# Kernel tuning notes

Hardware: AMD Instinct MI355X
Metric: run time of the kernel (lower is better)

## Reference

```python
import jax, jax.numpy as jnp
import numpy as np

B, T, H, NH, EL = 64, 1024, 256, 4, 768
DH = H // NH
EPS = 1e-3


def _ln(x, g, b):
    mu = jnp.mean(x, axis=-1, keepdims=True)
    var = jnp.var(x, axis=-1, keepdims=True)
    return (x - mu) * jax.lax.rsqrt(var + EPS) * g + b


def _glu(x, W, b):
    y = x @ W.T + b
    a, gate = jnp.split(y, 2, axis=-1)
    return a * jax.nn.sigmoid(gate)


def setup_inputs() -> dict:
    key = jax.random.key(0)
    ks = iter(jax.random.split(key, 40))
    w = lambda *s: jax.random.normal(next(ks), s, jnp.float32) * 0.02
    inp = {
        "temporal_features": jax.random.normal(next(ks), (B, T, H), jnp.float32),
        "ce": jax.random.normal(next(ks), (B, H), jnp.float32),
        # enrichment GRN (with context)
        "eg_Wa": w(H, H), "eg_ba": jnp.zeros((H,), jnp.float32),
        "eg_Wc": w(H, H),
        "eg_Wi": w(H, H), "eg_bi": jnp.zeros((H,), jnp.float32),
        "eg_Wg": w(2 * H, H), "eg_bg": jnp.zeros((2 * H,), jnp.float32),
        "eg_lng": jnp.ones((H,), jnp.float32), "eg_lnb": jnp.zeros((H,), jnp.float32),
        # interpretable MHA
        "att_Wqkv": w((2 * NH + 1) * DH, H),
        "att_Wout": w(H, DH),
        # attention gate + LN
        "ag_W": w(2 * H, H), "ag_b": jnp.zeros((2 * H,), jnp.float32),
        "aln_g": jnp.ones((H,), jnp.float32), "aln_b": jnp.zeros((H,), jnp.float32),
        # positionwise GRN (no context)
        "pg_Wa": w(H, H), "pg_ba": jnp.zeros((H,), jnp.float32),
        "pg_Wi": w(H, H), "pg_bi": jnp.zeros((H,), jnp.float32),
        "pg_Wg": w(2 * H, H), "pg_bg": jnp.zeros((2 * H,), jnp.float32),
        "pg_lng": jnp.ones((H,), jnp.float32), "pg_lnb": jnp.zeros((H,), jnp.float32),
        # decoder gate + LN
        "dg_W": w(2 * H, H), "dg_b": jnp.zeros((2 * H,), jnp.float32),
        "dln_g": jnp.ones((H,), jnp.float32), "dln_b": jnp.zeros((H,), jnp.float32),
    }
    return inp


def _forward(temporal_features, ce,
             eg_Wa, eg_ba, eg_Wc, eg_Wi, eg_bi, eg_Wg, eg_bg, eg_lng, eg_lnb,
             att_Wqkv, att_Wout,
             ag_W, ag_b, aln_g, aln_b,
             pg_Wa, pg_ba, pg_Wi, pg_bi, pg_Wg, pg_bg, pg_lng, pg_lnb,
             dg_W, dg_b, dln_g, dln_b):
    # enrichment GRN: linear + context -> ELU -> linear -> GLU -> residual -> LN
    x = temporal_features @ eg_Wa.T + eg_ba + (ce @ eg_Wc.T)[:, None, :]
    x = jax.nn.elu(x)
    x = x @ eg_Wi.T + eg_bi
    x = _glu(x, eg_Wg, eg_bg)
    enriched = _ln(x + temporal_features, eg_lng, eg_lnb)

    # interpretable multi-head attention (shared V, head-averaged output)
    qkv = enriched @ att_Wqkv.T  # [B,T,(2*NH+1)*DH]
    q = qkv[..., : NH * DH].reshape(B, T, NH, DH)
    k = qkv[..., NH * DH: 2 * NH * DH].reshape(B, T, NH, DH)
    v = qkv[..., 2 * NH * DH:]  # [B,T,DH]
    scale = DH ** -0.5
    scores = jnp.einsum("bthd,bshd->bhts", q, k) * scale  # [B,NH,T,T]
    mask = jnp.triu(jnp.full((T, T), -jnp.inf, jnp.float32), k=1)
    probs = jax.nn.softmax(scores + mask, axis=-1)
    attn_vec = jnp.einsum("bhts,bsd->bhtd", probs, v)  # [B,NH,T,DH]
    m_attn = jnp.mean(attn_vec, axis=1)  # [B,T,DH]
    a = m_attn @ att_Wout.T  # [B,T,H]

    # slice to decoder steps
    a = a[:, EL:, :]
    tf_dec = temporal_features[:, EL:, :]
    enr_dec = enriched[:, EL:, :]

    x = _glu(a, ag_W, ag_b)
    x = _ln(x + enr_dec, aln_g, aln_b)

    # positionwise GRN
    y = jax.nn.elu(x @ pg_Wa.T + pg_ba)
    y = y @ pg_Wi.T + pg_bi
    y = _glu(y, pg_Wg, pg_bg)
    x = _ln(y + x, pg_lng, pg_lnb)

    x = _glu(x, dg_W, dg_b)
    x = _ln(x + tf_dec, dln_g, dln_b)
    return x


def reference(temporal_features, ce,
              eg_Wa, eg_ba, eg_Wc, eg_Wi, eg_bi, eg_Wg, eg_bg, eg_lng, eg_lnb,
              att_Wqkv, att_Wout,
              ag_W, ag_b, aln_g, aln_b,
              pg_Wa, pg_ba, pg_Wi, pg_bi, pg_Wg, pg_bg, pg_lng, pg_lnb,
              dg_W, dg_b, dln_g, dln_b):
    return _forward(temporal_features, ce,
                    eg_Wa, eg_ba, eg_Wc, eg_Wi, eg_bi, eg_Wg, eg_bg, eg_lng, eg_lnb,
                    att_Wqkv, att_Wout,
                    ag_W, ag_b, aln_g, aln_b,
                    pg_Wa, pg_ba, pg_Wi, pg_bi, pg_Wg, pg_bg, pg_lng, pg_lnb,
                    dg_W, dg_b, dln_g, dln_b)
```

## Files before the change

### kernel.cpp

```cpp
#include <hip/hip_runtime.h>
#include <hip/hip_bf16.h>
#include <math.h>

typedef __hip_bfloat16 bf16;
typedef unsigned short u16;
typedef unsigned int u32;
typedef __attribute__((ext_vector_type(8))) short bfrag8;
typedef __attribute__((ext_vector_type(8))) _Float16 hfrag8;
typedef __attribute__((ext_vector_type(4))) float f32x4;

constexpr int Bb = 64, Tt = 1024, Hh = 256, NHn = 4, DHd = 64, ELe = 768;
constexpr int TD = Tt - ELe;
constexpr int BT = Bb * Tt;
constexpr int BD = Bb * TD;

__device__ __forceinline__ bool probe_bf16(const void* probe) {
    return *(const unsigned int*)probe == 0x3F803F80u;
}
__device__ __forceinline__ float bfbits2f(unsigned short u) {
    union { unsigned int i; float f; } c; c.i = ((unsigned int)u) << 16; return c.f;
}
__device__ __forceinline__ u16 f2bf(float f) {
    union { float f; unsigned int u; } c; c.f = f;
    unsigned int r = c.u + 0x7fffu + ((c.u >> 16) & 1u);
    return (u16)(r >> 16);
}
__device__ __forceinline__ u16 f2h(float f) {
    union { _Float16 h; u16 u; } c; c.h = (_Float16)f; return c.u;
}
__device__ __forceinline__ float h2f(u16 u) {
    union { u16 u; _Float16 h; } c; c.u = u; return (float)c.h;
}
__device__ __forceinline__ float4 load4dt(const void* p, long idx, bool bf) {
    if (bf) {
        ushort4 u = *(const ushort4*)((const unsigned short*)p + idx);
        return make_float4(bfbits2f(u.x), bfbits2f(u.y), bfbits2f(u.z), bfbits2f(u.w));
    }
    return *(const float4*)((const float*)p + idx);
}
__device__ __forceinline__ float load1dt(const void* p, long idx, bool bf) {
    return bf ? bfbits2f(((const unsigned short*)p)[idx]) : ((const float*)p)[idx];
}
__device__ __forceinline__ int swz(int row, int k) {
    return row * 64 + ((((k >> 3) ^ (row & 7)) << 3) | (k & 7));
}
__device__ __forceinline__ void gload16(const void* g, void* l) {
    __builtin_amdgcn_global_load_lds(
        (const __attribute__((address_space(1))) void*)g,
        (__attribute__((address_space(3))) void*)l, 16, 0, 0);
}
__device__ __forceinline__ u32 pkbf(float a, float b) {
    return (u32)f2bf(a) | ((u32)f2bf(b) << 16);
}

__global__ __launch_bounds__(256) void cvt_f16(const void* __restrict__ src,
                                               u16* __restrict__ dst,
                                               long n4, const void* __restrict__ probe)
{
    const bool dtb = probe_bf16(probe);
    long i = (long)blockIdx.x * 256 + threadIdx.x;
    long stride = (long)gridDim.x * 256;
    for (; i < n4; i += stride) {
        float4 v = load4dt(src, i * 4, dtb);
        ushort4 o = make_ushort4(f2h(v.x), f2h(v.y), f2h(v.z), f2h(v.w));
        *(ushort4*)&dst[i * 4] = o;
    }
}

__global__ __launch_bounds__(256) void cvtw_all(
    const void* s0, const void* s1, const void* s2, const void* s3,
    const void* s4, const void* s5, const void* s6, const void* s7,
    const void* s8, const void* s9, u16* __restrict__ dst,
    const void* __restrict__ probe)
{
    const bool dtb = probe_bf16(probe);
    int blk = blockIdx.x;
    const void* src; long seg0, base;
    if      (blk < 64)  { src = s0; seg0 = 0;   base = 0;      }
    else if (blk < 128) { src = s1; seg0 = 64;  base = 65536;  }
    else if (blk < 256) { src = s2; seg0 = 128; base = 131072; }
    else if (blk < 400) { src = s3; seg0 = 256; base = 262144; }
    else if (blk < 416) { src = s4; seg0 = 400; base = 409600; }
    else if (blk < 544) { src = s5; seg0 = 416; base = 425984; }
    else if (blk < 608) { src = s6; seg0 = 544; base = 557056; }
    else if (blk < 672) { src = s7; seg0 = 608; base = 622592; }
    else if (blk < 800) { src = s8; seg0 = 672; base = 688128; }
    else                { src = s9; seg0 = 800; base = 819200; }
    long i = (long)(blk - seg0) * 1024 + (long)threadIdx.x * 4;
    float4 v = load4dt(src, i, dtb);
    ushort4 o = make_ushort4(f2h(v.x), f2h(v.y), f2h(v.z), f2h(v.w));
    *(ushort4*)&dst[base + i] = o;
}

__global__ __launch_bounds__(256) void ceproj_kernel(const void* __restrict__ ce,
                                                     const void* __restrict__ Wc,
                                                     const void* __restrict__ probe,
                                                     float* __restrict__ out)
{
    const bool bf = probe_bf16(probe);
    __shared__ float ces[256];
    int b = blockIdx.x, tid = threadIdx.x;
    ces[tid] = load1dt(ce, b * 256 + tid, bf);
    __syncthreads();
    float acc = 0.f;
    #pragma unroll 4
    for (int k = 0; k < 256; k += 4) {
        float4 w4 = load4dt(Wc, (long)tid * 256 + k, bf);
        acc = fmaf(ces[k], w4.x, acc);
        acc = fmaf(ces[k + 1], w4.y, acc);
        acc = fmaf(ces[k + 2], w4.z, acc);
        acc = fmaf(ces[k + 3], w4.w, acc);
    }
    out[b * 256 + tid] = acc;
}

__global__ __launch_bounds__(256, 3) void gemm_mfma(
    const u16* __restrict__ A_g, const u16* __restrict__ W_g,
    const void* __restrict__ bias,
    const float* __restrict__ ceproj,
    const void* __restrict__ res0,
    void* __restrict__ Cout,
    const void* __restrict__ probe,
    int M, int N, int K, int mode,
    int res_kind, int a_decmap, int res_decmap, int out_kind)
{
    const int tid = threadIdx.x;
    const int w = tid >> 6, lane = tid & 63, lr = lane & 15, lg = lane >> 4;
    const int wm = w >> 1, wn = w & 1;
    const int m0 = blockIdx.x * 128;
    const int n0 = blockIdx.y * 128;
    const int n0g = blockIdx.y * 64;

    __shared__ __align__(16) u16 AsF[128 * 64];
    __shared__ __align__(16) u16 WsF[128 * 64];

    const int sl8 = lane >> 3;
    const int slot = lane & 7;

    long aoff[4]; int wrow[4];
    #pragma unroll
    for (int i = 0; i < 4; ++i) {
        int row = w * 32 + i * 8 + sl8;
        int gm = m0 + row;
        long ar = a_decmap ? ((long)(gm >> 8) * 1024 + 768 + (gm & 255)) : (long)gm;
        aoff[i] = ar * K + (long)((slot ^ (row & 7)) * 8);
        int wr;
        if (mode == 3) {
            int g = row >> 5;
            wr = ((g & 1) ? 256 : 0) + n0g + ((g >> 1) << 5) + (row & 31);
        } else {
            wr = n0 + row; if (wr > N - 1) wr = N - 1;
        }
        wrow[i] = wr;
    }

    f32x4 acc[4][4];
    #pragma unroll
    for (int i = 0; i < 4; ++i)
        #pragma unroll
        for (int j = 0; j < 4; ++j) acc[i][j] = (f32x4){0.f, 0.f, 0.f, 0.f};

    for (int kt = 0; kt < K; kt += 64) {
        __syncthreads();
        #pragma unroll
        for (int i = 0; i < 4; ++i) {
            int rbase = w * 32 + i * 8;
            gload16(A_g + aoff[i] + kt, &AsF[rbase * 64]);
            int row = rbase + sl8;
            gload16(W_g + (long)wrow[i] * K + kt + (slot ^ (row & 7)) * 8,
                    &WsF[rbase * 64]);
        }
        __syncthreads();

        #pragma unroll
        for (int kh = 0; kh < 2; ++kh) {
            hfrag8 wf[4];
            #pragma unroll
            for (int j = 0; j < 4; ++j)
                wf[j] = *(const hfrag8*)&WsF[swz(wn * 64 + j * 16 + lr, kh * 32 + lg * 8)];
            #pragma unroll
            for (int i = 0; i < 4; ++i) {
                hfrag8 ah = *(const hfrag8*)&AsF[swz(wm * 64 + i * 16 + lr, kh * 32 + lg * 8)];
                #pragma unroll
                for (int j = 0; j < 4; ++j)
                    acc[i][j] = __builtin_amdgcn_mfma_f32_16x16x32_f16(ah, wf[j], acc[i][j], 0, 0, 0);
            }
        }
    }

    const bool dtb = probe_bf16(probe);
    #pragma unroll
    for (int i = 0; i < 4; ++i) {
        #pragma unroll
        for (int r = 0; r < 4; ++r) {
            int gm = m0 + wm * 64 + i * 16 + lg * 4 + r;
            if (mode == 3) {
                long rrow = res_decmap ? ((long)(gm >> 8) * 1024 + 768 + (gm & 255)) : (long)gm;
                #pragma unroll
                for (int jj = 0; jj < 2; ++jj) {
                    int c = n0g + wn * 32 + jj * 16 + lr;
                    float a = acc[i][jj][r]     + load1dt(bias, c, dtb);
                    float g = acc[i][jj + 2][r] + load1dt(bias, c + 256, dtb);
                    float rv;
                    if (res_kind == 1) rv = h2f(((const u16*)res0)[rrow * 256 + c]);
                    else               rv = load1dt(res0, rrow * 256 + c, dtb);
                    float o = a / (1.f + expf(-g)) + rv;
                    long ci = (long)gm * 256 + c;
                    if (out_kind == 2) ((u16*)Cout)[ci] = f2h(o);
                    else               ((float*)Cout)[ci] = o;
                }
            } else {
                #pragma unroll
                for (int j = 0; j < 4; ++j) {
                    int n = n0 + wn * 64 + j * 16 + lr;
                    if (n < N) {
                        float v = acc[i][j][r];
                        if (bias) v += load1dt(bias, n, dtb);
                        if (mode == 1) v += ceproj[((gm >> 10) << 8) + n];
                        if (mode >= 1) v = (v > 0.f) ? v : expm1f(v);
                        long ci = (long)gm * N + n;
                        if (out_kind == 0)      ((float*)Cout)[ci] = v;
                        else if (out_kind == 1) ((u16*)Cout)[ci] = f2bf(v);
                        else                    ((u16*)Cout)[ci] = f2h(v);
                    }
                }
            }
        }
    }
}

__global__ __launch_bounds__(256) void ln_kernel(const u16* __restrict__ vin,
                                                 const void* __restrict__ g,
                                                 const void* __restrict__ beta,
                                                 void* __restrict__ out,
                                                 const void* __restrict__ probe,
                                                 int out_kind)
{
    const bool dtb = probe_bf16(probe);
    int tid = threadIdx.x;
    long m = (long)blockIdx.x * 4 + (tid >> 6);
    int l = tid & 63;
    ushort4 raw = *(const ushort4*)&vin[m * 256 + l * 4];
    float v0 = h2f(raw.x), v1 = h2f(raw.y), v2 = h2f(raw.z), v3 = h2f(raw.w);
    float s  = v0 + v1 + v2 + v3;
    float s2 = v0 * v0 + v1 * v1 + v2 * v2 + v3 * v3;
    #pragma unroll
    for (int off = 32; off > 0; off >>= 1) {
        s  += __shfl_xor(s, off);
        s2 += __shfl_xor(s2, off);
    }
    float mu  = s * (1.f / 256.f);
    float var = s2 * (1.f / 256.f) - mu * mu;
    float rstd = rsqrtf(var + 1e-3f);
    float4 gg = load4dt(g, l * 4, dtb);
    float4 bb = load4dt(beta, l * 4, dtb);
    float y0 = (v0 - mu) * rstd * gg.x + bb.x;
    float y1 = (v1 - mu) * rstd * gg.y + bb.y;
    float y2 = (v2 - mu) * rstd * gg.z + bb.z;
    float y3 = (v3 - mu) * rstd * gg.w + bb.w;
    long idx = m * 256 + l * 4;
    if (out_kind == 2) {
        *(ushort4*)&((u16*)out)[idx] = make_ushort4(f2h(y0), f2h(y1), f2h(y2), f2h(y3));
    } else if (dtb) {
        *(ushort4*)&((u16*)out)[idx] = make_ushort4(f2bf(y0), f2bf(y1), f2bf(y2), f2bf(y3));
    } else {
        *(float4*)&((float*)out)[idx] = make_float4(y0, y1, y2, y3);
    }
}

__global__ __launch_bounds__(256) void vtrans(const u16* __restrict__ vtmp,
                                              u16* __restrict__ vt)
{
    int b  = blockIdx.x >> 4;
    int s0 = (blockIdx.x & 15) << 6;
    __shared__ u16 t[64][72];
    int tid = threadIdx.x;
    {
        int sl = tid >> 4;
        int d0 = (tid & 15) << 2;
        #pragma unroll
        for (int u = 0; u < 4; ++u) {
            int s = u * 16 + sl;
            ushort4 v4 = *(const ushort4*)&vtmp[((long)(b * 1024 + s0 + s)) * 64 + d0];
            t[d0 + 0][s] = v4.x; t[d0 + 1][s] = v4.y;
            t[d0 + 2][s] = v4.z; t[d0 + 3][s] = v4.w;
        }
    }
    __syncthreads();
    {
        int d = tid >> 2, c0 = (tid & 3) << 4;
        u16* dst = vt + ((long)(b * 64 + d)) * 1024 + s0 + c0;
        *(uint4*)dst       = *(const uint4*)&t[d][c0];
        *(uint4*)(dst + 8) = *(const uint4*)&t[d][c0 + 8];
    }
}

__global__ __launch_bounds__(256) void attn_mfma(const u16* __restrict__ qd,
                                                 const u16* __restrict__ kb,
                                                 const u16* __restrict__ vt,
                                                 float* __restrict__ Oscr)
{
    int bid = blockIdx.x;
    int qt = bid & 3, h = (bid >> 2) & 3, b = bid >> 4;
    int tid = threadIdx.x;
    int w = tid >> 6, lane = tid & 63, lr = lane & 15, lg = lane >> 4;

    __shared__ u16 Ks[64][72];
    __shared__ u16 Vs[64][72];

    bfrag8 qf0, qf1;
    {
        long tok = (long)b * 256 + qt * 64 + w * 16 + lr;
        const u16* qp = qd + tok * 256 + h * 64 + lg * 8;
        qf0 = *(const bfrag8*)(qp);
        qf1 = *(const bfrag8*)(qp + 32);
    }

    f32x4 O[4];
    float m_i = -INFINITY, l_i = 0.f;
    #pragma unroll
    for (int jd = 0; jd < 4; ++jd) O[jd] = (f32x4){0.f, 0.f, 0.f, 0.f};
    const int qabs = 768 + qt * 64 + w * 16 + lr;

    const int srcA = lr + ((lg & 1) ? 32 : 0);
    const int srcB = srcA + 16;
    const bool hi = (lg >= 2);

    const int ntiles = 13 + qt;
    for (int st = 0; st < ntiles; ++st) {
        int s0 = st * 64;
        __syncthreads();
        {
            int row = tid >> 2, c0 = (tid & 3) << 4;
            const u16* kp = kb + ((long)(b * 1024 + s0 + row)) * 256 + h * 64 + c0;
            *(uint4*)&Ks[row][c0]     = *(const uint4*)kp;
            *(uint4*)&Ks[row][c0 + 8] = *(const uint4*)(kp + 8);
            const u16* vp = vt + ((long)(b * 64 + row)) * 1024 + s0 + c0;
            *(uint4*)&Vs[row][c0]     = *(const uint4*)vp;
            *(uint4*)&Vs[row][c0 + 8] = *(const uint4*)(vp + 8);
        }
        __syncthreads();

        f32x4 sv[4];
        #pragma unroll
        for (int jb = 0; jb < 4; ++jb) {
            f32x4 a = (f32x4){0.f, 0.f, 0.f, 0.f};
            a = __builtin_amdgcn_mfma_f32_16x16x32_bf16(
                    *(const bfrag8*)&Ks[jb * 16 + lr][lg * 8], qf0, a, 0, 0, 0);
            a = __builtin_amdgcn_mfma_f32_16x16x32_bf16(
                    *(const bfrag8*)&Ks[jb * 16 + lr][32 + lg * 8], qf1, a, 0, 0, 0);
            sv[jb] = a;
        }

        const bool lastt = (st == ntiles - 1);
        #pragma unroll
        for (int jb = 0; jb < 4; ++jb)
            #pragma unroll
            for (int r = 0; r < 4; ++r) {
                float x = sv[jb][r] * 0.125f;
                if (lastt && (s0 + jb * 16 + lg * 4 + r > qabs)) x = -INFINITY;
                sv[jb][r] = x;
            }

        float mx = -INFINITY;
        #pragma unroll
        for (int jb = 0; jb < 4; ++jb)
            #pragma unroll
            for (int r = 0; r < 4; ++r) mx = fmaxf(mx, sv[jb][r]);
        mx = fmaxf(mx, __shfl_xor(mx, 16));
        mx = fmaxf(mx, __shfl_xor(mx, 32));
        float mnew = fmaxf(m_i, mx);
        float alpha = __expf(m_i - mnew);
        float ps = 0.f;
        #pragma unroll
        for (int jb = 0; jb < 4; ++jb)
            #pragma unroll
            for (int r = 0; r < 4; ++r) {
                float p = __expf(sv[jb][r] - mnew);
                sv[jb][r] = p; ps += p;
            }
        ps += __shfl_xor(ps, 16);
        ps += __shfl_xor(ps, 32);
        l_i = l_i * alpha + ps;
        m_i = mnew;

        float alr[4];
        #pragma unroll
        for (int r = 0; r < 4; ++r) alr[r] = __shfl(alpha, lg * 4 + r);
        #pragma unroll
        for (int jd = 0; jd < 4; ++jd)
            #pragma unroll
            for (int r = 0; r < 4; ++r) O[jd][r] *= alr[r];

        u32 c0_[2], c1_[2], c2_[2], c3_[2];
        c0_[0] = pkbf(sv[0][0], sv[0][1]); c0_[1] = pkbf(sv[0][2], sv[0][3]);
        c1_[0] = pkbf(sv[1][0], sv[1][1]); c1_[1] = pkbf(sv[1][2], sv[1][3]);
        c2_[0] = pkbf(sv[2][0], sv[2][1]); c2_[1] = pkbf(sv[2][2], sv[2][3]);
        c3_[0] = pkbf(sv[3][0], sv[3][1]); c3_[1] = pkbf(sv[3][2], sv[3][3]);

        #pragma unroll
        for (int sh = 0; sh < 2; ++sh) {
            u32 lo0 = sh ? c2_[0] : c0_[0], lo1 = sh ? c2_[1] : c0_[1];
            u32 hi0 = sh ? c3_[0] : c1_[0], hi1 = sh ? c3_[1] : c1_[1];
            u32 a0 = (u32)__shfl((int)lo0, srcA), a1 = (u32)__shfl((int)lo1, srcA);
            u32 A0 = (u32)__shfl((int)hi0, srcA), A1 = (u32)__shfl((int)hi1, srcA);
            u32 b0 = (u32)__shfl((int)lo0, srcB), b1 = (u32)__shfl((int)lo1, srcB);
            u32 B0 = (u32)__shfl((int)hi0, srcB), B1 = (u32)__shfl((int)hi1, srcB);
            union { u32 u[4]; bfrag8 v; } pu;
            pu.u[0] = hi ? A0 : a0; pu.u[1] = hi ? A1 : a1;
            pu.u[2] = hi ? B0 : b0; pu.u[3] = hi ? B1 : b1;
            #pragma unroll
            for (int jd = 0; jd < 4; ++jd) {
                bfrag8 vb = *(const bfrag8*)&Vs[jd * 16 + lr][sh * 32 + lg * 8];
                O[jd] = __builtin_amdgcn_mfma_f32_16x16x32_bf16(pu.v, vb, O[jd], 0, 0, 0);
            }
        }
    }

    float inv = 1.f / l_i;
    float linv[4];
    #pragma unroll
    for (int r = 0; r < 4; ++r) linv[r] = __shfl(inv, lg * 4 + r);
    #pragma unroll
    for (int jd = 0; jd < 4; ++jd)
        #pragma unroll
        for (int r = 0; r < 4; ++r) {
            long token = (long)b * 256 + qt * 64 + w * 16 + lg * 4 + r;
            Oscr[token * 256 + h * 64 + jd * 16 + lr] = O[jd][r] * linv[r];
        }
}

__global__ __launch_bounds__(256) void headmean(const float* __restrict__ O,
                                                u16* __restrict__ outH)
{
    int i = blockIdx.x * 256 + threadIdx.x;
    int token = i >> 6, d = i & 63;
    const float* p = O + (long)token * 256 + d;
    float m = 0.25f * (p[0] + p[64] + p[128] + p[192]);
    outH[i] = f2h(m);
}

extern "C" void kernel_launch(void* const* d_in, const int* in_sizes, int n_in,
                              void* d_out, int out_size, void* d_ws, size_t ws_size,
                              hipStream_t stream)
{
    const void* tf       = d_in[0];
    const void* ce       = d_in[1];
    const void* eg_Wa    = d_in[2];
    const void* eg_ba    = d_in[3];
    const void* eg_Wc    = d_in[4];
    const void* eg_Wi    = d_in[5];
    const void* eg_bi    = d_in[6];
    const void* eg_Wg    = d_in[7];
    const void* eg_bg    = d_in[8];
    const void* eg_lng   = d_in[9];
    const void* eg_lnb   = d_in[10];
    const void* att_Wqkv = d_in[11];
    const void* att_Wout = d_in[12];
    const void* ag_W     = d_in[13];
    const void* ag_b     = d_in[14];
    const void* aln_g    = d_in[15];
    const void* aln_b    = d_in[16];
    const void* pg_Wa    = d_in[17];
    const void* pg_ba    = d_in[18];
    const void* pg_Wi    = d_in[19];
    const void* pg_bi    = d_in[20];
    const void* pg_Wg    = d_in[21];
    const void* pg_bg    = d_in[22];
    const void* pg_lng   = d_in[23];
    const void* pg_lnb   = d_in[24];
    const void* dg_W     = d_in[25];
    const void* dg_b     = d_in[26];
    const void* dln_g    = d_in[27];
    const void* dln_b    = d_in[28];
    const void* probe    = eg_lng;

    float* ws = (float*)d_ws;

    const long CEP = 0;
    const long WPo = 65536;
    const long P   = 1114112;
    const long Q   = P + 8388608L;
    const long T   = Q + 16777216L;

    float* ceprojF = ws + CEP;

    u16* wp = (u16*)(ws + WPo);
    const long nWa = 65536, nWi = 65536, nWg = 131072, nWqkv = 147456,
               nWout = 16384, nAg = 131072, nPa = 65536, nPi = 65536,
               nPg = 131072, nDg = 131072;
    u16* WaH = wp + 0;      u16* WiH = wp + 65536;  u16* WgH = wp + 131072;
    u16* WqH = wp + 262144; u16* WoH = wp + 409600; u16* AgH = wp + 425984;
    u16* PaH = wp + 557056; u16* PiH = wp + 622592; u16* PgH = wp + 688128;
    u16* DgH = wp + 819200;

    u16* tfH   = (u16*)(ws + P);
    u16* g1H   = (u16*)(ws + Q);
    u16* x2H   = (u16*)(ws + Q + 8388608L);
    u16* glu3H = (u16*)(ws + Q);
    u16* enrH  = (u16*)(ws + T);

    u16*   kvbK = (u16*)(ws + Q);
    u16*   vtmp = (u16*)(ws + Q + 8388608L);
    u16*   qd16 = (u16*)(ws + Q + 8388608L + 2097152L);
    u16*   vt16 = (u16*)(ws + Q + 8388608L + 4194304L);
    float* Oscr = ws + P;
    u16*   matnH = (u16*)(ws + P + 4194304L);

    u16* D[8];
    for (int k = 0; k < 8; ++k) D[k] = (u16*)(ws + Q + (long)k * 2097152L);

    dim3 blk(256);
    auto cgrid = [](long n4) {
        long g = (n4 + 255) / 256; if (g > 2048) g = 2048; return dim3((unsigned)g);
    };
    const long NBT = (long)BT * 256;

    cvt_f16<<<cgrid(NBT / 4), blk, 0, stream>>>(tf, tfH, NBT / 4, probe);
    cvtw_all<<<928, blk, 0, stream>>>(eg_Wa, eg_Wi, eg_Wg, att_Wqkv, att_Wout,
                                      ag_W, pg_Wa, pg_Wi, pg_Wg, dg_W, wp, probe);
    ceproj_kernel<<<64, blk, 0, stream>>>(ce, eg_Wc, probe, ceprojF);

    gemm_mfma<<<dim3(BT / 128, 2), blk, 0, stream>>>(
        tfH, WaH, eg_ba, ceprojF, nullptr, g1H, probe, BT, 256, 256, 1, 0, 0, 0, 2);
    gemm_mfma<<<dim3(BT / 128, 2), blk, 0, stream>>>(
        g1H, WiH, eg_bi, nullptr, nullptr, x2H, probe, BT, 256, 256, 0, 0, 0, 0, 2);
    gemm_mfma<<<dim3(BT / 128, 4), blk, 0, stream>>>(
        x2H, WgH, eg_bg, nullptr, tf, glu3H, probe, BT, 256, 256, 3, 0, 0, 0, 2);
    ln_kernel<<<BT / 4, blk, 0, stream>>>(glu3H, eg_lng, eg_lnb, enrH, probe, 2);

    gemm_mfma<<<dim3(BT / 128, 2), blk, 0, stream>>>(
        enrH, WqH + (long)256 * 256, nullptr, nullptr, nullptr, kvbK, probe,
        BT, 256, 256, 0, 0, 0, 0, 1);
    gemm_mfma<<<dim3(BT / 128, 1), blk, 0, stream>>>(
        enrH, WqH + (long)512 * 256, nullptr, nullptr, nullptr, vtmp, probe,
        BT, 64, 256, 0, 0, 0, 0, 1);
    gemm_mfma<<<dim3(BD / 128, 2), blk, 0, stream>>>(
        enrH, WqH, nullptr, nullptr, nullptr, qd16, probe,
        BD, 256, 256, 0, 0, 1, 0, 1);
    vtrans<<<1024, blk, 0, stream>>>(vtmp, vt16);

    attn_mfma<<<Bb * NHn * 4, blk, 0, stream>>>(qd16, kvbK, vt16, Oscr);
    headmean<<<(BD * 64) / 256, blk, 0, stream>>>(Oscr, matnH);

    gemm_mfma<<<dim3(BD / 128, 2), blk, 0, stream>>>(
        matnH, WoH, nullptr, nullptr, nullptr, D[0], probe, BD, 256, 64, 0, 0, 0, 0, 2);
    gemm_mfma<<<dim3(BD / 128, 4), blk, 0, stream>>>(
        D[0], AgH, ag_b, nullptr, enrH, D[1], probe, BD, 256, 256, 3, 1, 0, 1, 2);
    ln_kernel<<<BD / 4, blk, 0, stream>>>(D[1], aln_g, aln_b, D[2], probe, 2);
    gemm_mfma<<<dim3(BD / 128, 2), blk, 0, stream>>>(
        D[2], PaH, pg_ba, nullptr, nullptr, D[3], probe, BD, 256, 256, 2, 0, 0, 0, 2);
    gemm_mfma<<<dim3(BD / 128, 2), blk, 0, stream>>>(
        D[3], PiH, pg_bi, nullptr, nullptr, D[4], probe, BD, 256, 256, 0, 0, 0, 0, 2);
    gemm_mfma<<<dim3(BD / 128, 4), blk, 0, stream>>>(
        D[4], PgH, pg_bg, nullptr, D[2], D[5], probe, BD, 256, 256, 3, 1, 0, 0, 2);
    ln_kernel<<<BD / 4, blk, 0, stream>>>(D[5], pg_lng, pg_lnb, D[6], probe, 2);
    gemm_mfma<<<dim3(BD / 128, 4), blk, 0, stream>>>(
        D[6], DgH, dg_b, nullptr, tf, D[7], probe, BD, 256, 256, 3, 0, 0, 1, 2);
    ln_kernel<<<BD / 4, blk, 0, stream>>>(D[7], dln_g, dln_b, d_out, probe, 1);
}
```

Baseline: 573.3 us.

## Double-buffer LDS tiles in GEMM and attention, fold softmax scale into Q

Gemm and attention kernels now prefetch the next K tile into a second LDS buffer with direct global-to-LDS loads while computing on the current one, halving barriers per step. The attention K/V tiles switch to an XOR-swizzled layout. The softmax scale times log2(e) is applied when writing Q, so attention uses exp2 without a per-element multiply. Fast exp intrinsics and a hardware packed bf16 conversion replace slower paths, while doubled LDS lowers occupancy to two blocks.

```diff
diff --git a/kernel.cpp b/kernel.cpp
--- a/kernel.cpp
+++ b/kernel.cpp
@@ -13,6 +13,7 @@
 constexpr int TD = Tt - ELe;
 constexpr int BT = Bb * Tt;
 constexpr int BD = Bb * TD;
+constexpr float QSCALE = 0.18033688011112042f;
 
 __device__ __forceinline__ bool probe_bf16(const void* probe) {
     return *(const unsigned int*)probe == 0x3F803F80u;
@@ -49,8 +50,8 @@
         (const __attribute__((address_space(1))) void*)g,
         (__attribute__((address_space(3))) void*)l, 16, 0, 0);
 }
-__device__ __forceinline__ u32 pkbf(float a, float b) {
-    return (u32)f2bf(a) | ((u32)f2bf(b) << 16);
+__device__ __forceinline__ u32 cvtpk(float a, float b) {
+    u32 r; asm("v_cvt_pk_bf16_f32 %0, %1, %2" : "=v"(r) : "v"(a), "v"(b)); return r;
 }
 
 __global__ __launch_bounds__(256) void cvt_f16(const void* __restrict__ src,
@@ -114,7 +115,7 @@
     out[b * 256 + tid] = acc;
 }
 
-__global__ __launch_bounds__(256, 3) void gemm_mfma(
+__global__ __launch_bounds__(256, 2) void gemm_mfma(
     const u16* __restrict__ A_g, const u16* __restrict__ W_g,
     const void* __restrict__ bias,
     const float* __restrict__ ceproj,
@@ -131,13 +132,13 @@
     const int n0 = blockIdx.y * 128;
     const int n0g = blockIdx.y * 64;
 
-    __shared__ __align__(16) u16 AsF[128 * 64];
-    __shared__ __align__(16) u16 WsF[128 * 64];
+    __shared__ __align__(16) u16 AsF[2][128 * 64];
+    __shared__ __align__(16) u16 WsF[2][128 * 64];
 
     const int sl8 = lane >> 3;
     const int slot = lane & 7;
 
-    long aoff[4]; int wrow[4];
+    long aoff[4]; long woff[4];
     #pragma unroll
     for (int i = 0; i < 4; ++i) {
         int row = w * 32 + i * 8 + sl8;
@@ -151,7 +152,7 @@
         } else {
             wr = n0 + row; if (wr > N - 1) wr = N - 1;
         }
-        wrow[i] = wr;
+        woff[i] = (long)wr * K + (long)((slot ^ (row & 7)) * 8);
     }
 
     f32x4 acc[4][4];
@@ -160,32 +161,39 @@
         #pragma unroll
         for (int j = 0; j < 4; ++j) acc[i][j] = (f32x4){0.f, 0.f, 0.f, 0.f};
 
+    #pragma unroll
+    for (int i = 0; i < 4; ++i) {
+        int rbase = w * 32 + i * 8;
+        gload16(A_g + aoff[i], &AsF[0][rbase * 64]);
+        gload16(W_g + woff[i], &WsF[0][rbase * 64]);
+    }
+
+    int cur = 0;
     for (int kt = 0; kt < K; kt += 64) {
         __syncthreads();
-        #pragma unroll
-        for (int i = 0; i < 4; ++i) {
-            int rbase = w * 32 + i * 8;
-            gload16(A_g + aoff[i] + kt, &AsF[rbase * 64]);
-            int row = rbase + sl8;
-            gload16(W_g + (long)wrow[i] * K + kt + (slot ^ (row & 7)) * 8,
-                    &WsF[rbase * 64]);
-        }
-        __syncthreads();
-
+        if (kt + 64 < K) {
+            #pragma unroll
+            for (int i = 0; i < 4; ++i) {
+                int rbase = w * 32 + i * 8;
+                gload16(A_g + aoff[i] + kt + 64, &AsF[cur ^ 1][rbase * 64]);
+                gload16(W_g + woff[i] + kt + 64, &WsF[cur ^ 1][rbase * 64]);
+            }
+        }
         #pragma unroll
         for (int kh = 0; kh < 2; ++kh) {
             hfrag8 wf[4];
             #pragma unroll
             for (int j = 0; j < 4; ++j)
-                wf[j] = *(const hfrag8*)&WsF[swz(wn * 64 + j * 16 + lr, kh * 32 + lg * 8)];
+                wf[j] = *(const hfrag8*)&WsF[cur][swz(wn * 64 + j * 16 + lr, kh * 32 + lg * 8)];
             #pragma unroll
             for (int i = 0; i < 4; ++i) {
-                hfrag8 ah = *(const hfrag8*)&AsF[swz(wm * 64 + i * 16 + lr, kh * 32 + lg * 8)];
+                hfrag8 ah = *(const hfrag8*)&AsF[cur][swz(wm * 64 + i * 16 + lr, kh * 32 + lg * 8)];
                 #pragma unroll
                 for (int j = 0; j < 4; ++j)
                     acc[i][j] = __builtin_amdgcn_mfma_f32_16x16x32_f16(ah, wf[j], acc[i][j], 0, 0, 0);
             }
         }
+        cur ^= 1;
     }
 
     const bool dtb = probe_bf16(probe);
@@ -204,7 +212,7 @@
                     float rv;
                     if (res_kind == 1) rv = h2f(((const u16*)res0)[rrow * 256 + c]);
                     else               rv = load1dt(res0, rrow * 256 + c, dtb);
-                    float o = a / (1.f + expf(-g)) + rv;
+                    float o = a / (1.f + __expf(-g)) + rv;
                     long ci = (long)gm * 256 + c;
                     if (out_kind == 2) ((u16*)Cout)[ci] = f2h(o);
                     else               ((float*)Cout)[ci] = o;
@@ -217,10 +225,11 @@
                         float v = acc[i][j][r];
                         if (bias) v += load1dt(bias, n, dtb);
                         if (mode == 1) v += ceproj[((gm >> 10) << 8) + n];
-                        if (mode >= 1) v = (v > 0.f) ? v : expm1f(v);
+                        if (mode >= 1) v = (v > 0.f) ? v : (__expf(v) - 1.f);
                         long ci = (long)gm * N + n;
                         if (out_kind == 0)      ((float*)Cout)[ci] = v;
                         else if (out_kind == 1) ((u16*)Cout)[ci] = f2bf(v);
+                        else if (out_kind == 3) ((u16*)Cout)[ci] = f2bf(v * QSCALE);
                         else                    ((u16*)Cout)[ci] = f2h(v);
                     }
                 }
@@ -304,9 +313,10 @@
     int qt = bid & 3, h = (bid >> 2) & 3, b = bid >> 4;
     int tid = threadIdx.x;
     int w = tid >> 6, lane = tid & 63, lr = lane & 15, lg = lane >> 4;
-
-    __shared__ u16 Ks[64][72];
-    __shared__ u16 Vs[64][72];
+    const int sl8 = lane >> 3, slot = lane & 7;
+
+    __shared__ __align__(16) u16 Ks[2][64 * 64];
+    __shared__ __align__(16) u16 Vs[2][64 * 64];
 
     bfrag8 qf0, qf1;
     {
@@ -325,42 +335,54 @@
     const int srcA = lr + ((lg & 1) ? 32 : 0);
     const int srcB = srcA + 16;
     const bool hi = (lg >= 2);
-
     const int ntiles = 13 + qt;
+
+    const long kbase = (long)b * 1024 * 256 + h * 64;
+    const long vbase = (long)b * 64 * 1024;
+
+    #pragma unroll
+    for (int i = 0; i < 2; ++i) {
+        int rbase = w * 16 + i * 8;
+        int row = rbase + sl8;
+        int sw = (slot ^ (row & 7)) * 8;
+        gload16(kb + kbase + (long)row * 256 + sw, &Ks[0][rbase * 64]);
+        gload16(vt + vbase + (long)row * 1024 + sw, &Vs[0][rbase * 64]);
+    }
+
+    int cur = 0;
     for (int st = 0; st < ntiles; ++st) {
         int s0 = st * 64;
         __syncthreads();
-        {
-            int row = tid >> 2, c0 = (tid & 3) << 4;
-            const u16* kp = kb + ((long)(b * 1024 + s0 + row)) * 256 + h * 64 + c0;
-            *(uint4*)&Ks[row][c0]     = *(const uint4*)kp;
-            *(uint4*)&Ks[row][c0 + 8] = *(const uint4*)(kp + 8);
-            const u16* vp = vt + ((long)(b * 64 + row)) * 1024 + s0 + c0;
-            *(uint4*)&Vs[row][c0]     = *(const uint4*)vp;
-            *(uint4*)&Vs[row][c0 + 8] = *(const uint4*)(vp + 8);
-        }
-        __syncthreads();
+        if (st + 1 < ntiles) {
+            int s1 = s0 + 64;
+            #pragma unroll
+            for (int i = 0; i < 2; ++i) {
+                int rbase = w * 16 + i * 8;
+                int row = rbase + sl8;
+                int sw = (slot ^ (row & 7)) * 8;
+                gload16(kb + kbase + (long)(s1 + row) * 256 + sw, &Ks[cur ^ 1][rbase * 64]);
+                gload16(vt + vbase + (long)row * 1024 + s1 + sw, &Vs[cur ^ 1][rbase * 64]);
+            }
+        }
 
         f32x4 sv[4];
         #pragma unroll
         for (int jb = 0; jb < 4; ++jb) {
             f32x4 a = (f32x4){0.f, 0.f, 0.f, 0.f};
             a = __builtin_amdgcn_mfma_f32_16x16x32_bf16(
-                    *(const bfrag8*)&Ks[jb * 16 + lr][lg * 8], qf0, a, 0, 0, 0);
+                    *(const bfrag8*)&Ks[cur][swz(jb * 16 + lr, lg * 8)], qf0, a, 0, 0, 0);
             a = __builtin_amdgcn_mfma_f32_16x16x32_bf16(
-                    *(const bfrag8*)&Ks[jb * 16 + lr][32 + lg * 8], qf1, a, 0, 0, 0);
+                    *(const bfrag8*)&Ks[cur][swz(jb * 16 + lr, 32 + lg * 8)], qf1, a, 0, 0, 0);
             sv[jb] = a;
         }
 
-        const bool lastt = (st == ntiles - 1);
-        #pragma unroll
-        for (int jb = 0; jb < 4; ++jb)
-            #pragma unroll
-            for (int r = 0; r < 4; ++r) {
-                float x = sv[jb][r] * 0.125f;
-                if (lastt && (s0 + jb * 16 + lg * 4 + r > qabs)) x = -INFINITY;
-                sv[jb][r] = x;
-            }
+        if (st == ntiles - 1) {
+            #pragma unroll
+            for (int jb = 0; jb < 4; ++jb)
+                #pragma unroll
+                for (int r = 0; r < 4; ++r)
+                    if (s0 + jb * 16 + lg * 4 + r > qabs) sv[jb][r] = -INFINITY;
+        }
 
         float mx = -INFINITY;
         #pragma unroll
@@ -370,13 +392,13 @@
         mx = fmaxf(mx, __shfl_xor(mx, 16));
         mx = fmaxf(mx, __shfl_xor(mx, 32));
         float mnew = fmaxf(m_i, mx);
-        float alpha = __expf(m_i - mnew);
+        float alpha = exp2f(m_i - mnew);
         float ps = 0.f;
         #pragma unroll
         for (int jb = 0; jb < 4; ++jb)
             #pragma unroll
             for (int r = 0; r < 4; ++r) {
-                float p = __expf(sv[jb][r] - mnew);
+                float p = exp2f(sv[jb][r] - mnew);
                 sv[jb][r] = p; ps += p;
             }
         ps += __shfl_xor(ps, 16);
@@ -393,10 +415,10 @@
             for (int r = 0; r < 4; ++r) O[jd][r] *= alr[r];
 
         u32 c0_[2], c1_[2], c2_[2], c3_[2];
-        c0_[0] = pkbf(sv[0][0], sv[0][1]); c0_[1] = pkbf(sv[0][2], sv[0][3]);
-        c1_[0] = pkbf(sv[1][0], sv[1][1]); c1_[1] = pkbf(sv[1][2], sv[1][3]);
-        c2_[0] = pkbf(sv[2][0], sv[2][1]); c2_[1] = pkbf(sv[2][2], sv[2][3]);
-        c3_[0] = pkbf(sv[3][0], sv[3][1]); c3_[1] = pkbf(sv[3][2], sv[3][3]);
+        c0_[0] = cvtpk(sv[0][0], sv[0][1]); c0_[1] = cvtpk(sv[0][2], sv[0][3]);
+        c1_[0] = cvtpk(sv[1][0], sv[1][1]); c1_[1] = cvtpk(sv[1][2], sv[1][3]);
+        c2_[0] = cvtpk(sv[2][0], sv[2][1]); c2_[1] = cvtpk(sv[2][2], sv[2][3]);
+        c3_[0] = cvtpk(sv[3][0], sv[3][1]); c3_[1] = cvtpk(sv[3][2], sv[3][3]);
 
         #pragma unroll
         for (int sh = 0; sh < 2; ++sh) {
@@ -411,10 +433,11 @@
             pu.u[2] = hi ? B0 : b0; pu.u[3] = hi ? B1 : b1;
             #pragma unroll
             for (int jd = 0; jd < 4; ++jd) {
-                bfrag8 vb = *(const bfrag8*)&Vs[jd * 16 + lr][sh * 32 + lg * 8];
+                bfrag8 vb = *(const bfrag8*)&Vs[cur][swz(jd * 16 + lr, sh * 32 + lg * 8)];
                 O[jd] = __builtin_amdgcn_mfma_f32_16x16x32_bf16(pu.v, vb, O[jd], 0, 0, 0);
             }
         }
+        cur ^= 1;
     }
 
     float inv = 1.f / l_i;
@@ -486,9 +509,6 @@
     float* ceprojF = ws + CEP;
 
     u16* wp = (u16*)(ws + WPo);
-    const long nWa = 65536, nWi = 65536, nWg = 131072, nWqkv = 147456,
-               nWout = 16384, nAg = 131072, nPa = 65536, nPi = 65536,
-               nPg = 131072, nDg = 131072;
     u16* WaH = wp + 0;      u16* WiH = wp + 65536;  u16* WgH = wp + 131072;
     u16* WqH = wp + 262144; u16* WoH = wp + 409600; u16* AgH = wp + 425984;
     u16* PaH = wp + 557056; u16* PiH = wp + 622592; u16* PgH = wp + 688128;
@@ -537,7 +557,7 @@
         BT, 64, 256, 0, 0, 0, 0, 1);
     gemm_mfma<<<dim3(BD / 128, 2), blk, 0, stream>>>(
         enrH, WqH, nullptr, nullptr, nullptr, qd16, probe,
-        BD, 256, 256, 0, 0, 1, 0, 1);
+        BD, 256, 256, 0, 0, 1, 0, 3);
     vtrans<<<1024, blk, 0, stream>>>(vtmp, vt16);
 
     attn_mfma<<<Bb * NHn * 4, blk, 0, stream>>>(qd16, kvbK, vt16, Oscr);
```

Result: slower. 655.9 us (+14.4%).
